# Kernel tuning notes

Hardware: AMD Instinct MI355X
Metric: run time of the kernel (lower is better)

## Reference

```python
import jax, jax.numpy as jnp
import numpy as np

# Dims
B, S, D = 2, 2048, 1024
H, KV = 16, 4            # rosa heads / kv heads -> n_rep = 4
QKB, VB = 16, 32          # query-key bits / value bits
N_REP = H // KV
TAU = 1.0


def setup_inputs() -> dict:
    key = jax.random.key(0)
    ks = jax.random.split(key, 8)
    sc = lambda fan_in: 1.0 / np.sqrt(fan_in)
    return {
        "hidden_states": jax.random.normal(ks[0], (B, S, D), jnp.float32),
        # Linear weights stored (in, out) so y = x @ W
        "Wq": jax.random.normal(ks[1], (D, H * QKB), jnp.float32) * sc(D),
        "Wk": jax.random.normal(ks[2], (D, KV * QKB), jnp.float32) * sc(D),
        "Wv": jax.random.normal(ks[3], (D, KV * VB), jnp.float32) * sc(D),
        "Wo": jax.random.normal(ks[4], (H * VB, D), jnp.float32) * sc(H * VB),
        "v_emb0": jnp.full((H * VB,), -1e-05, jnp.float32),
        "v_emb1": jnp.full((H * VB,), +1e-05, jnp.float32),
    }


def _repeat_kv(x, n_rep):
    # x: [B, KV, S, d] -> [B, KV*n_rep, S, d]
    b, kv, s, d = x.shape
    return jnp.broadcast_to(x[:, :, None], (b, kv, n_rep, s, d)).reshape(b, kv * n_rep, s, d)


def reference(hidden_states, Wq, Wk, Wv, Wo, v_emb0, v_emb1):
    b, s, _ = hidden_states.shape
    q = (hidden_states @ Wq).reshape(b, s, H, QKB).transpose(0, 2, 1, 3)   # [B,H,S,QKB]
    k = (hidden_states @ Wk).reshape(b, s, KV, QKB).transpose(0, 2, 1, 3)
    v = (hidden_states @ Wv).reshape(b, s, KV, VB).transpose(0, 2, 1, 3)
    k = _repeat_kv(k, N_REP)                                               # [B,H,S,QKB]
    v = _repeat_kv(v, N_REP)                                               # [B,H,S,VB]

    # Soft binarization (hard path uses (x > 0); soft path relaxes with sigmoid(x/tau)).
    pq = jax.nn.sigmoid(q / TAU)
    pk = jax.nn.sigmoid(k / TAU)
    pv = jax.nn.sigmoid(v / TAU)

    # Expected number of matching bits between soft-binary q_i and k_j:
    # sum_b [ pq*pk + (1-pq)(1-pk) ] = QKB - sum(pq) - sum(pk) + 2 * pq.pk
    dot = jnp.einsum("bhsd,bhtd->bhst", pq, pk)                            # [B,H,S,S]
    scores = QKB - pq.sum(-1)[:, :, :, None] - pk.sum(-1)[:, :, None, :] + 2.0 * dot

    causal = jnp.tril(jnp.ones((s, s), bool))                              # [S,S]
    scores = jnp.where(causal[None, None], scores, jnp.finfo(scores.dtype).min)
    attn = jax.nn.softmax(scores / TAU, axis=-1)

    vh = jnp.einsum("bhst,bhtd->bhsd", attn, pv)                           # [B,H,S,VB]
    e0 = v_emb0.reshape(1, H, 1, VB)
    e1 = v_emb1.reshape(1, H, 1, VB)
    out = e0 * (1.0 - vh) + e1 * vh                                        # [B,H,S,VB]
    out = out.transpose(0, 2, 1, 3).reshape(b, s, H * VB)
    return out @ Wo                                                        # [B,S,D]
```

## Files before the change

### kernel.cpp

```cpp
#include <hip/hip_runtime.h>
#include <hip/hip_bf16.h>

#define B_    2
#define S_    2048
#define D_    1024
#define H_    16
#define KV_   4
#define QKB_  16
#define VB_   32
#define NTOK  (B_ * S_)
#define L2E_  1.44269504088896f

typedef __attribute__((ext_vector_type(8))) short bshort8;
typedef __attribute__((ext_vector_type(4))) float f32x4;

__device__ __forceinline__ unsigned short bf16_rne(float x) {
    unsigned u = __float_as_uint(x);
    return (unsigned short)((u + 0x7FFFu + ((u >> 16) & 1u)) >> 16);
}
__device__ __forceinline__ unsigned bf16x2_rne(float lo, float hi) {
    return (unsigned)bf16_rne(lo) | ((unsigned)bf16_rne(hi) << 16);
}
__device__ __forceinline__ unsigned cvt_pk_bf16(float lo, float hi) {
    unsigned r;
    asm("v_cvt_pk_bf16_f32 %0, %1, %2" : "=v"(r) : "v"(lo), "v"(hi));
    return r;
}
__device__ __forceinline__ float sum2bf(unsigned u) {
    return __uint_as_float(u << 16) + __uint_as_float(u & 0xFFFF0000u);
}
__device__ __forceinline__ void stage16(const unsigned short* g, unsigned short* l) {
    __builtin_amdgcn_global_load_lds(
        (const __attribute__((address_space(1))) void*)g,
        (__attribute__((address_space(3))) void*)l, 16, 0, 0);
}

__global__ __launch_bounds__(256) void prep_kernel(
    const float* __restrict__ hs,
    const float* __restrict__ Wq, const float* __restrict__ Wk,
    const float* __restrict__ Wv, const float* __restrict__ Wo,
    unsigned short* __restrict__ hs_b,
    unsigned short* __restrict__ Wcat_t, unsigned short* __restrict__ Wot)
{
    __shared__ float T[64][65];
    const int t = threadIdx.x;
    if (blockIdx.x < 2048) {
        int i = blockIdx.x * 256 + t;
        const float4* s = (const float4*)hs;
        float4 a = s[2 * i], b = s[2 * i + 1];
        uint4 o;
        o.x = bf16x2_rne(a.x, a.y); o.y = bf16x2_rne(a.z, a.w);
        o.z = bf16x2_rne(b.x, b.y); o.w = bf16x2_rne(b.z, b.w);
        ((uint4*)hs_b)[i] = o;
        return;
    }
    const int bid = blockIdx.x - 2048;
    const float* src; unsigned short* dst; int K, N, tk, tn, drow0;
    if (bid < 64)       { src = Wq; dst = Wcat_t; K = 1024; N = 256;  int r = bid;       tk = r & 15; tn = r >> 4; drow0 = 0; }
    else if (bid < 80)  { src = Wk; dst = Wcat_t; K = 1024; N = 64;   int r = bid - 64;  tk = r;      tn = 0;      drow0 = 256; }
    else if (bid < 112) { src = Wv; dst = Wcat_t; K = 1024; N = 128;  int r = bid - 80;  tk = r & 15; tn = r >> 4; drow0 = 320; }
    else                { src = Wo; dst = Wot;    K = 512;  N = 1024; int r = bid - 112; tk = r & 7;  tn = r >> 3; drow0 = 0; }
    const int k0 = tk * 64, n0 = tn * 64;
    const int rr = t >> 4, cc = (t & 15) * 4;
    #pragma unroll
    for (int i = 0; i < 4; ++i) {
        float4 v = *(const float4*)(src + (k0 + rr + i * 16) * N + n0 + cc);
        T[rr + i * 16][cc + 0] = v.x; T[rr + i * 16][cc + 1] = v.y;
        T[rr + i * 16][cc + 2] = v.z; T[rr + i * 16][cc + 3] = v.w;
    }
    __syncthreads();
    const int nloc = t >> 2, kc = (t & 3) * 16;
    unsigned o[8];
    #pragma unroll
    for (int j = 0; j < 8; ++j)
        o[j] = bf16x2_rne(T[kc + 2 * j][nloc], T[kc + 2 * j + 1][nloc]);
    unsigned short* dp = dst + (drow0 + n0 + nloc) * K + k0 + kc;
    uint4 w0; w0.x = o[0]; w0.y = o[1]; w0.z = o[2]; w0.w = o[3];
    uint4 w1; w1.x = o[4]; w1.y = o[5]; w1.z = o[6]; w1.w = o[7];
    *(uint4*)(dp) = w0;
    *(uint4*)(dp + 8) = w1;
}

__global__ __launch_bounds__(256, 4) void proj_gemm(
    const unsigned short* __restrict__ Ab, const unsigned short* __restrict__ Btb,
    unsigned short* __restrict__ qg, unsigned short* __restrict__ pko,
    unsigned short* __restrict__ pvT)
{
    __shared__ unsigned short As[64 * 64];
    __shared__ unsigned short Bs[64 * 64];
    const int tid = threadIdx.x, l = tid & 63, w = tid >> 6;
    const int l15 = l & 15, quad = l >> 4;
    const int m0 = blockIdx.x * 64, n0 = blockIdx.y * 64;
    const int sr8 = l >> 3, sc8 = l & 7;
    f32x4 c[4];
    #pragma unroll
    for (int j = 0; j < 4; ++j) c[j] = (f32x4){0.f, 0.f, 0.f, 0.f};

    for (int k0 = 0; k0 < 1024; k0 += 64) {
        int R0 = w * 8, r0 = R0 + sr8;
        int R1 = 32 + w * 8, r1 = R1 + sr8;
        stage16(Ab  + (m0 + r0) * 1024 + k0 + (sc8 ^ (r0 & 7)) * 8, &As[R0 * 64]);
        stage16(Ab  + (m0 + r1) * 1024 + k0 + (sc8 ^ (r1 & 7)) * 8, &As[R1 * 64]);
        stage16(Btb + (n0 + r0) * 1024 + k0 + (sc8 ^ (r0 & 7)) * 8, &Bs[R0 * 64]);
        stage16(Btb + (n0 + r1) * 1024 + k0 + (sc8 ^ (r1 & 7)) * 8, &Bs[R1 * 64]);
        __syncthreads();
        #pragma unroll
        for (int kh = 0; kh < 2; ++kh) {
            const int arow = w * 16 + l15;
            bshort8 a = *(const bshort8*)&As[arow * 64 + (((kh * 4 + quad) ^ (arow & 7)) * 8)];
            #pragma unroll
            for (int bc = 0; bc < 4; ++bc) {
                const int brow = bc * 16 + l15;
                bshort8 b = *(const bshort8*)&Bs[brow * 64 + (((kh * 4 + quad) ^ (brow & 7)) * 8)];
                c[bc] = __builtin_amdgcn_mfma_f32_16x16x32_bf16(a, b, c[bc], 0, 0, 0);
            }
        }
        __syncthreads();
    }

    const int tok0 = m0 + w * 16 + quad * 4;
    #pragma unroll
    for (int bc = 0; bc < 4; ++bc) {
        f32x4 v = c[bc];
        const int n = n0 + bc * 16 + l15;
        float sg[4];
        #pragma unroll
        for (int r = 0; r < 4; ++r)
            sg[r] = 1.f / (1.f + exp2f(-v[r] * L2E_));
        if (n < 256) {
            const int hh = n >> 4, d = n & 15;
            #pragma unroll
            for (int r = 0; r < 4; ++r) {
                int tok = tok0 + r, bb = tok >> 11, ss = tok & 2047;
                qg[(((bb * 16 + hh) * 2048) + ss) * 16 + d] =
                    bf16_rne(L2E_ * (2.f * sg[r] - 1.f));
            }
        } else if (n < 320) {
            const int j = n - 256, kvv = j >> 4, d = j & 15;
            #pragma unroll
            for (int r = 0; r < 4; ++r) {
                int tok = tok0 + r, bb = tok >> 11, ss = tok & 2047;
                pko[(((bb * 4 + kvv) * 2048) + ss) * 16 + d] = bf16_rne(sg[r]);
            }
        } else {
            const int j = n - 320, kvv = j >> 5, d = j & 31;
            const int bb = tok0 >> 11, ss = tok0 & 2047;
            const int tl = ss >> 6, ccol = ss & 63;
            uint2 wv; wv.x = bf16x2_rne(sg[0], sg[1]); wv.y = bf16x2_rne(sg[2], sg[3]);
            *(uint2*)(pvT + ((((bb * 4 + kvv) * 32) + tl) * 32 + d) * 64 + ccol) = wv;
        }
    }
}

__global__ __launch_bounds__(256, 2) void outproj_gemm(
    const unsigned short* __restrict__ Ab, const unsigned short* __restrict__ Btb,
    float* __restrict__ out)
{
    __shared__ unsigned short As[64 * 64];
    __shared__ unsigned short Bs[128 * 64];
    const int tid = threadIdx.x, l = tid & 63, w = tid >> 6;
    const int l15 = l & 15, quad = l >> 4;
    const int m0 = blockIdx.x * 64, n0 = blockIdx.y * 128;
    const int wr = w & 1, wc = w >> 1;
    const int sr8 = l >> 3, sc8 = l & 7;
    f32x4 c[2][4];
    #pragma unroll
    for (int i = 0; i < 2; ++i)
        #pragma unroll
        for (int j = 0; j < 4; ++j) c[i][j] = (f32x4){0.f, 0.f, 0.f, 0.f};

    for (int k0 = 0; k0 < 512; k0 += 64) {
        #pragma unroll
        for (int j = 0; j < 2; ++j) {
            int R = w * 16 + j * 8, r = R + sr8;
            stage16(Ab + (m0 + r) * 512 + k0 + (sc8 ^ (r & 7)) * 8, &As[R * 64]);
        }
        #pragma unroll
        for (int j = 0; j < 4; ++j) {
            int R = j * 32 + w * 8, r = R + sr8;
            stage16(Btb + (n0 + r) * 512 + k0 + (sc8 ^ (r & 7)) * 8, &Bs[R * 64]);
        }
        __syncthreads();
        #pragma unroll
        for (int kh = 0; kh < 2; ++kh) {
            bshort8 a[2], b[4];
            #pragma unroll
            for (int ar = 0; ar < 2; ++ar) {
                int row = wr * 32 + ar * 16 + l15;
                a[ar] = *(const bshort8*)&As[row * 64 + (((kh * 4 + quad) ^ (row & 7)) * 8)];
            }
            #pragma unroll
            for (int bc = 0; bc < 4; ++bc) {
                int row = wc * 64 + bc * 16 + l15;
                b[bc] = *(const bshort8*)&Bs[row * 64 + (((kh * 4 + quad) ^ (row & 7)) * 8)];
            }
            #pragma unroll
            for (int ar = 0; ar < 2; ++ar)
                #pragma unroll
                for (int bc = 0; bc < 4; ++bc)
                    c[ar][bc] = __builtin_amdgcn_mfma_f32_16x16x32_bf16(a[ar], b[bc], c[ar][bc], 0, 0, 0);
        }
        __syncthreads();
    }

    #pragma unroll
    for (int ar = 0; ar < 2; ++ar)
        #pragma unroll
        for (int bc = 0; bc < 4; ++bc) {
            f32x4 v = c[ar][bc];
            const int col = n0 + wc * 64 + bc * 16 + l15;
            const int r0 = m0 + wr * 32 + ar * 16 + quad * 4;
            #pragma unroll
            for (int r = 0; r < 4; ++r)
                out[(r0 + r) * D_ + col] = v[r];
        }
}

__global__ __launch_bounds__(256, 4) void attn_kernel(
    const unsigned short* __restrict__ qg_g, const unsigned short* __restrict__ pk_g,
    const unsigned short* __restrict__ pvT_g, const float* __restrict__ e0,
    const float* __restrict__ e1, unsigned short* __restrict__ xo)
{
    __shared__ unsigned short P[4][16][88];
    const int tid = threadIdx.x, l = tid & 63, wq = tid >> 6;
    const int l15 = l & 15, quad = l >> 4;
    const int g = blockIdx.x;
    const int idx = g & 255, kg = g >> 8;
    const int bh = idx & 31, rr = idx >> 5;
    int qt;
    if      (kg == 0) qt = rr;
    else if (kg == 1) qt = 31 - rr;
    else if (kg == 2) qt = 8 + rr;
    else              qt = 23 - rr;
    const int b = bh >> 4, h = bh & 15, kv = h >> 2;
    const int qbase = qt * 64;
    const unsigned short* pkb = pk_g + ((b * 4 + kv) * 2048) * 16;
    const unsigned short* pvb = pvT_g + (b * 4 + kv) * 65536;
    const unsigned short* qgb = qg_g + ((b * 16 + h) * 2048) * 16;

    const f32x4 zero4 = {0.f, 0.f, 0.f, 0.f};
    const bshort8 zero8 = {0, 0, 0, 0, 0, 0, 0, 0};

    const unsigned short* qrow = qgb + (qbase + wq * 16 + l15) * 16;
    uint4 qu0 = *(const uint4*)qrow;
    uint4 qu1 = *(const uint4*)(qrow + 8);
    float s = sum2bf(qu0.x) + sum2bf(qu0.y) + sum2bf(qu0.z) + sum2bf(qu0.w)
            + sum2bf(qu1.x) + sum2bf(qu1.y) + sum2bf(qu1.z) + sum2bf(qu1.w);
    bshort8 qfrag = zero8;
    if (quad == 0)      qfrag = __builtin_bit_cast(bshort8, qu0);
    else if (quad == 1) qfrag = __builtin_bit_cast(bshort8, qu1);
    else if (quad == 2) qfrag[0] = (short)bf16_rne(-8.f * L2E_ - 0.5f * s);

    bshort8 kone = zero8; kone[0] = (short)0x3F80;

    f32x4 acc0 = zero4, acc1 = zero4;
    float lsum = 0.f;

    bshort8 kc[4], vc[4], kn[4], vn[4];
    if (quad < 2) {
        #pragma unroll
        for (int ks = 0; ks < 4; ++ks)
            kc[ks] = *(const bshort8*)(pkb + (ks * 16 + l15) * 16 + quad * 8);
    }
    {
        const unsigned short* vb = pvb + l15 * 64 + quad * 8;
        vc[0] = *(const bshort8*)(vb);
        vc[1] = *(const bshort8*)(vb + 32);
        vc[2] = *(const bshort8*)(vb + 1024);
        vc[3] = *(const bshort8*)(vb + 1056);
    }

    #pragma unroll 2
    for (int t = 0; t < qt; ++t) {
        if (quad < 2) {
            #pragma unroll
            for (int ks = 0; ks < 4; ++ks)
                kn[ks] = *(const bshort8*)(pkb + ((t + 1) * 64 + ks * 16 + l15) * 16 + quad * 8);
        }
        {
            const unsigned short* vb = pvb + (t + 1) * 2048 + l15 * 64 + quad * 8;
            vn[0] = *(const bshort8*)(vb);
            vn[1] = *(const bshort8*)(vb + 32);
            vn[2] = *(const bshort8*)(vb + 1024);
            vn[3] = *(const bshort8*)(vb + 1056);
        }
        f32x4 sc[4];
        #pragma unroll
        for (int ks = 0; ks < 4; ++ks) {
            bshort8 kf;
            if (quad < 2)       kf = kc[ks];
            else if (quad == 2) kf = kone;
            else                kf = zero8;
            sc[ks] = __builtin_amdgcn_mfma_f32_16x16x32_bf16(kf, qfrag, zero4, 0, 0, 0);
        }
        #pragma unroll
        for (int ks = 0; ks < 4; ++ks) {
            float p0 = exp2f(sc[ks][0]), p1 = exp2f(sc[ks][1]);
            float p2 = exp2f(sc[ks][2]), p3 = exp2f(sc[ks][3]);
            lsum += p0 + p1 + p2 + p3;
            uint2 wv; wv.x = cvt_pk_bf16(p0, p1); wv.y = cvt_pk_bf16(p2, p3);
            *(uint2*)&P[wq][l15][ks * 16 + quad * 4] = wv;
        }
        {
            bshort8 pf0 = *(const bshort8*)&P[wq][l15][quad * 8];
            bshort8 pf1 = *(const bshort8*)&P[wq][l15][32 + quad * 8];
            acc0 = __builtin_amdgcn_mfma_f32_16x16x32_bf16(vc[0], pf0, acc0, 0, 0, 0);
            acc1 = __builtin_amdgcn_mfma_f32_16x16x32_bf16(vc[2], pf0, acc1, 0, 0, 0);
            acc0 = __builtin_amdgcn_mfma_f32_16x16x32_bf16(vc[1], pf1, acc0, 0, 0, 0);
            acc1 = __builtin_amdgcn_mfma_f32_16x16x32_bf16(vc[3], pf1, acc1, 0, 0, 0);
        }
        #pragma unroll
        for (int i = 0; i < 4; ++i) { kc[i] = kn[i]; vc[i] = vn[i]; }
    }

    {
        const int t0 = qt * 64;
        const int q_lane = qbase + wq * 16 + l15;
        f32x4 sc[4];
        #pragma unroll
        for (int ks = 0; ks < 4; ++ks) {
            bshort8 kf;
            if (quad < 2)       kf = kc[ks];
            else if (quad == 2) kf = kone;
            else                kf = zero8;
            sc[ks] = __builtin_amdgcn_mfma_f32_16x16x32_bf16(kf, qfrag, zero4, 0, 0, 0);
        }
        #pragma unroll
        for (int ks = 0; ks < 4; ++ks) {
            float pv0[4];
            #pragma unroll
            for (int r = 0; r < 4; ++r) {
                const int tg = t0 + ks * 16 + quad * 4 + r;
                float pp = (tg <= q_lane) ? exp2f(sc[ks][r]) : 0.f;
                lsum += pp; pv0[r] = pp;
            }
            uint2 wv; wv.x = cvt_pk_bf16(pv0[0], pv0[1]); wv.y = cvt_pk_bf16(pv0[2], pv0[3]);
            *(uint2*)&P[wq][l15][ks * 16 + quad * 4] = wv;
        }
        {
            bshort8 pf0 = *(const bshort8*)&P[wq][l15][quad * 8];
            bshort8 pf1 = *(const bshort8*)&P[wq][l15][32 + quad * 8];
            acc0 = __builtin_amdgcn_mfma_f32_16x16x32_bf16(vc[0], pf0, acc0, 0, 0, 0);
            acc1 = __builtin_amdgcn_mfma_f32_16x16x32_bf16(vc[2], pf0, acc1, 0, 0, 0);
            acc0 = __builtin_amdgcn_mfma_f32_16x16x32_bf16(vc[1], pf1, acc0, 0, 0, 0);
            acc1 = __builtin_amdgcn_mfma_f32_16x16x32_bf16(vc[3], pf1, acc1, 0, 0, 0);
        }
    }

    lsum += __shfl_xor(lsum, 16);
    lsum += __shfl_xor(lsum, 32);
    const float inv = 1.f / lsum;

    float e0v[8], dEv[8];
    #pragma unroll
    for (int vs = 0; vs < 2; ++vs)
        #pragma unroll
        for (int r = 0; r < 4; ++r) {
            int idx2 = h * 32 + vs * 16 + quad * 4 + r;
            float a = e0[idx2];
            e0v[vs * 4 + r] = a; dEv[vs * 4 + r] = e1[idx2] - a;
        }
    const int tok = b * 2048 + qbase + wq * 16 + l15;
    float o0[4], o1[4];
    #pragma unroll
    for (int r = 0; r < 4; ++r) {
        o0[r] = e0v[r]     + dEv[r]     * (acc0[r] * inv);
        o1[r] = e0v[4 + r] + dEv[4 + r] * (acc1[r] * inv);
    }
    uint2 w0; w0.x = cvt_pk_bf16(o0[0], o0[1]); w0.y = cvt_pk_bf16(o0[2], o0[3]);
    uint2 w1; w1.x = cvt_pk_bf16(o1[0], o1[1]); w1.y = cvt_pk_bf16(o1[2], o1[3]);
    *(uint2*)(xo + tok * 512 + h * 32 + quad * 4)      = w0;
    *(uint2*)(xo + tok * 512 + h * 32 + 16 + quad * 4) = w1;
}

extern "C" void kernel_launch(void* const* d_in, const int* in_sizes, int n_in,
                              void* d_out, int out_size, void* d_ws, size_t ws_size,
                              hipStream_t stream)
{
    const float* hs = (const float*)d_in[0];
    const float* Wq = (const float*)d_in[1];
    const float* Wk = (const float*)d_in[2];
    const float* Wv = (const float*)d_in[3];
    const float* Wo = (const float*)d_in[4];
    const float* e0 = (const float*)d_in[5];
    const float* e1 = (const float*)d_in[6];
    float* out = (float*)d_out;

    char* ws = (char*)d_ws;
    unsigned short* hs_b   = (unsigned short*)(ws);
    unsigned short* xo     = (unsigned short*)(ws);
    unsigned short* Wcat_t = (unsigned short*)(ws + 8388608);
    unsigned short* Wot    = (unsigned short*)(ws + 8388608 + 917504);
    unsigned short* qg     = (unsigned short*)(ws + 10354688);
    unsigned short* pk     = (unsigned short*)(ws + 12451840);
    unsigned short* pvT    = (unsigned short*)(ws + 12976128);

    prep_kernel<<<2288, 256, 0, stream>>>(hs, Wq, Wk, Wv, Wo, hs_b, Wcat_t, Wot);
    proj_gemm<<<dim3(64, 7), 256, 0, stream>>>(hs_b, Wcat_t, qg, pk, pvT);
    attn_kernel<<<1024, 256, 0, stream>>>(qg, pk, pvT, e0, e1, xo);
    outproj_gemm<<<dim3(64, 8), 256, 0, stream>>>(xo, Wot, out);
}
```

Baseline: 145.0 us.

## Split attention key range across two blocks and merge partials in finalize kernel

Each query tile's causal key range is divided into two halves processed by separate blocks, doubling the attention grid. Each block writes unnormalized fp32 accumulators and row sums to workspace. A new finalize kernel adds the two halves, normalizes, applies the value embeddings and writes bf16 output. This aims to improve load balance and parallelism, at the cost of extra global memory traffic for partials and an additional kernel launch.

```diff
diff --git a/kernel.cpp b/kernel.cpp
--- a/kernel.cpp
+++ b/kernel.cpp
@@ -218,20 +218,22 @@
 
 __global__ __launch_bounds__(256, 4) void attn_kernel(
     const unsigned short* __restrict__ qg_g, const unsigned short* __restrict__ pk_g,
-    const unsigned short* __restrict__ pvT_g, const float* __restrict__ e0,
-    const float* __restrict__ e1, unsigned short* __restrict__ xo)
+    const unsigned short* __restrict__ pvT_g,
+    float* __restrict__ pacc, float* __restrict__ plsum)
 {
     __shared__ unsigned short P[4][16][88];
     const int tid = threadIdx.x, l = tid & 63, wq = tid >> 6;
     const int l15 = l & 15, quad = l >> 4;
     const int g = blockIdx.x;
-    const int idx = g & 255, kg = g >> 8;
-    const int bh = idx & 31, rr = idx >> 5;
-    int qt;
-    if      (kg == 0) qt = rr;
-    else if (kg == 1) qt = 31 - rr;
-    else if (kg == 2) qt = 8 + rr;
-    else              qt = 23 - rr;
+    const int c = g & 255, j = g >> 8;
+    const int bh = c & 31, rr = c >> 5;
+    const int r = rr + ((j & 1) << 3);
+    const int hk = j >> 1;
+    const int qt = (hk & 2) ? (31 - r) : r;
+    const int half = hk & 1;
+    const int m = (qt + 1) >> 1;
+    const int kt0 = half ? m : 0;
+    const int nt  = half ? (qt - m) : m;
     const int b = bh >> 4, h = bh & 15, kv = h >> 2;
     const int qbase = qt * 64;
     const unsigned short* pkb = pk_g + ((b * 4 + kv) * 2048) * 16;
@@ -257,120 +259,140 @@
     float lsum = 0.f;
 
     bshort8 kc[4], vc[4], kn[4], vn[4];
-    if (quad < 2) {
-        #pragma unroll
-        for (int ks = 0; ks < 4; ++ks)
-            kc[ks] = *(const bshort8*)(pkb + (ks * 16 + l15) * 16 + quad * 8);
-    }
-    {
-        const unsigned short* vb = pvb + l15 * 64 + quad * 8;
-        vc[0] = *(const bshort8*)(vb);
-        vc[1] = *(const bshort8*)(vb + 32);
-        vc[2] = *(const bshort8*)(vb + 1024);
-        vc[3] = *(const bshort8*)(vb + 1056);
-    }
-
-    #pragma unroll 2
-    for (int t = 0; t < qt; ++t) {
+    if (nt > 0 || half) {
         if (quad < 2) {
             #pragma unroll
             for (int ks = 0; ks < 4; ++ks)
-                kn[ks] = *(const bshort8*)(pkb + ((t + 1) * 64 + ks * 16 + l15) * 16 + quad * 8);
+                kc[ks] = *(const bshort8*)(pkb + (kt0 * 64 + ks * 16 + l15) * 16 + quad * 8);
         }
         {
-            const unsigned short* vb = pvb + (t + 1) * 2048 + l15 * 64 + quad * 8;
-            vn[0] = *(const bshort8*)(vb);
-            vn[1] = *(const bshort8*)(vb + 32);
-            vn[2] = *(const bshort8*)(vb + 1024);
-            vn[3] = *(const bshort8*)(vb + 1056);
-        }
-        f32x4 sc[4];
-        #pragma unroll
-        for (int ks = 0; ks < 4; ++ks) {
-            bshort8 kf;
-            if (quad < 2)       kf = kc[ks];
-            else if (quad == 2) kf = kone;
-            else                kf = zero8;
-            sc[ks] = __builtin_amdgcn_mfma_f32_16x16x32_bf16(kf, qfrag, zero4, 0, 0, 0);
-        }
-        #pragma unroll
-        for (int ks = 0; ks < 4; ++ks) {
-            float p0 = exp2f(sc[ks][0]), p1 = exp2f(sc[ks][1]);
-            float p2 = exp2f(sc[ks][2]), p3 = exp2f(sc[ks][3]);
-            lsum += p0 + p1 + p2 + p3;
-            uint2 wv; wv.x = cvt_pk_bf16(p0, p1); wv.y = cvt_pk_bf16(p2, p3);
-            *(uint2*)&P[wq][l15][ks * 16 + quad * 4] = wv;
-        }
-        {
-            bshort8 pf0 = *(const bshort8*)&P[wq][l15][quad * 8];
-            bshort8 pf1 = *(const bshort8*)&P[wq][l15][32 + quad * 8];
-            acc0 = __builtin_amdgcn_mfma_f32_16x16x32_bf16(vc[0], pf0, acc0, 0, 0, 0);
-            acc1 = __builtin_amdgcn_mfma_f32_16x16x32_bf16(vc[2], pf0, acc1, 0, 0, 0);
-            acc0 = __builtin_amdgcn_mfma_f32_16x16x32_bf16(vc[1], pf1, acc0, 0, 0, 0);
-            acc1 = __builtin_amdgcn_mfma_f32_16x16x32_bf16(vc[3], pf1, acc1, 0, 0, 0);
-        }
-        #pragma unroll
-        for (int i = 0; i < 4; ++i) { kc[i] = kn[i]; vc[i] = vn[i]; }
-    }
-
-    {
-        const int t0 = qt * 64;
-        const int q_lane = qbase + wq * 16 + l15;
-        f32x4 sc[4];
-        #pragma unroll
-        for (int ks = 0; ks < 4; ++ks) {
-            bshort8 kf;
-            if (quad < 2)       kf = kc[ks];
-            else if (quad == 2) kf = kone;
-            else                kf = zero8;
-            sc[ks] = __builtin_amdgcn_mfma_f32_16x16x32_bf16(kf, qfrag, zero4, 0, 0, 0);
-        }
-        #pragma unroll
-        for (int ks = 0; ks < 4; ++ks) {
-            float pv0[4];
-            #pragma unroll
-            for (int r = 0; r < 4; ++r) {
-                const int tg = t0 + ks * 16 + quad * 4 + r;
-                float pp = (tg <= q_lane) ? exp2f(sc[ks][r]) : 0.f;
-                lsum += pp; pv0[r] = pp;
-            }
-            uint2 wv; wv.x = cvt_pk_bf16(pv0[0], pv0[1]); wv.y = cvt_pk_bf16(pv0[2], pv0[3]);
-            *(uint2*)&P[wq][l15][ks * 16 + quad * 4] = wv;
-        }
-        {
-            bshort8 pf0 = *(const bshort8*)&P[wq][l15][quad * 8];
-            bshort8 pf1 = *(const bshort8*)&P[wq][l15][32 + quad * 8];
-            acc0 = __builtin_amdgcn_mfma_f32_16x16x32_bf16(vc[0], pf0, acc0, 0, 0, 0);
-            acc1 = __builtin_amdgcn_mfma_f32_16x16x32_bf16(vc[2], pf0, acc1, 0, 0, 0);
-            acc0 = __builtin_amdgcn_mfma_f32_16x16x32_bf16(vc[1], pf1, acc0, 0, 0, 0);
-            acc1 = __builtin_amdgcn_mfma_f32_16x16x32_bf16(vc[3], pf1, acc1, 0, 0, 0);
+            const unsigned short* vb = pvb + kt0 * 2048 + l15 * 64 + quad * 8;
+            vc[0] = *(const bshort8*)(vb);
+            vc[1] = *(const bshort8*)(vb + 32);
+            vc[2] = *(const bshort8*)(vb + 1024);
+            vc[3] = *(const bshort8*)(vb + 1056);
+        }
+
+        #pragma unroll 2
+        for (int t = 0; t < nt; ++t) {
+            if (quad < 2) {
+                #pragma unroll
+                for (int ks = 0; ks < 4; ++ks)
+                    kn[ks] = *(const bshort8*)(pkb + ((kt0 + t + 1) * 64 + ks * 16 + l15) * 16 + quad * 8);
+            }
+            {
+                const unsigned short* vb = pvb + (kt0 + t + 1) * 2048 + l15 * 64 + quad * 8;
+                vn[0] = *(const bshort8*)(vb);
+                vn[1] = *(const bshort8*)(vb + 32);
+                vn[2] = *(const bshort8*)(vb + 1024);
+                vn[3] = *(const bshort8*)(vb + 1056);
+            }
+            f32x4 sc[4];
+            #pragma unroll
+            for (int ks = 0; ks < 4; ++ks) {
+                bshort8 kf;
+                if (quad < 2)       kf = kc[ks];
+                else if (quad == 2) kf = kone;
+                else                kf = zero8;
+                sc[ks] = __builtin_amdgcn_mfma_f32_16x16x32_bf16(kf, qfrag, zero4, 0, 0, 0);
+            }
+            #pragma unroll
+            for (int ks = 0; ks < 4; ++ks) {
+                float p0 = exp2f(sc[ks][0]), p1 = exp2f(sc[ks][1]);
+                float p2 = exp2f(sc[ks][2]), p3 = exp2f(sc[ks][3]);
+                lsum += p0 + p1 + p2 + p3;
+                uint2 wv; wv.x = cvt_pk_bf16(p0, p1); wv.y = cvt_pk_bf16(p2, p3);
+                *(uint2*)&P[wq][l15][ks * 16 + quad * 4] = wv;
+            }
+            {
+                bshort8 pf0 = *(const bshort8*)&P[wq][l15][quad * 8];
+                bshort8 pf1 = *(const bshort8*)&P[wq][l15][32 + quad * 8];
+                acc0 = __builtin_amdgcn_mfma_f32_16x16x32_bf16(vc[0], pf0, acc0, 0, 0, 0);
+                acc1 = __builtin_amdgcn_mfma_f32_16x16x32_bf16(vc[2], pf0, acc1, 0, 0, 0);
+                acc0 = __builtin_amdgcn_mfma_f32_16x16x32_bf16(vc[1], pf1, acc0, 0, 0, 0);
+                acc1 = __builtin_amdgcn_mfma_f32_16x16x32_bf16(vc[3], pf1, acc1, 0, 0, 0);
+            }
+            #pragma unroll
+            for (int i = 0; i < 4; ++i) { kc[i] = kn[i]; vc[i] = vn[i]; }
+        }
+
+        if (half) {
+            const int t0 = qt * 64;
+            const int q_lane = qbase + wq * 16 + l15;
+            f32x4 sc[4];
+            #pragma unroll
+            for (int ks = 0; ks < 4; ++ks) {
+                bshort8 kf;
+                if (quad < 2)       kf = kc[ks];
+                else if (quad == 2) kf = kone;
+                else                kf = zero8;
+                sc[ks] = __builtin_amdgcn_mfma_f32_16x16x32_bf16(kf, qfrag, zero4, 0, 0, 0);
+            }
+            #pragma unroll
+            for (int ks = 0; ks < 4; ++ks) {
+                float pv0[4];
+                #pragma unroll
+                for (int r2 = 0; r2 < 4; ++r2) {
+                    const int tg = t0 + ks * 16 + quad * 4 + r2;
+                    float pp = (tg <= q_lane) ? exp2f(sc[ks][r2]) : 0.f;
+                    lsum += pp; pv0[r2] = pp;
+                }
+                uint2 wv; wv.x = cvt_pk_bf16(pv0[0], pv0[1]); wv.y = cvt_pk_bf16(pv0[2], pv0[3]);
+                *(uint2*)&P[wq][l15][ks * 16 + quad * 4] = wv;
+            }
+            {
+                bshort8 pf0 = *(const bshort8*)&P[wq][l15][quad * 8];
+                bshort8 pf1 = *(const bshort8*)&P[wq][l15][32 + quad * 8];
+                acc0 = __builtin_amdgcn_mfma_f32_16x16x32_bf16(vc[0], pf0, acc0, 0, 0, 0);
+                acc1 = __builtin_amdgcn_mfma_f32_16x16x32_bf16(vc[2], pf0, acc1, 0, 0, 0);
+                acc0 = __builtin_amdgcn_mfma_f32_16x16x32_bf16(vc[1], pf1, acc0, 0, 0, 0);
+                acc1 = __builtin_amdgcn_mfma_f32_16x16x32_bf16(vc[3], pf1, acc1, 0, 0, 0);
+            }
         }
     }
 
     lsum += __shfl_xor(lsum, 16);
     lsum += __shfl_xor(lsum, 32);
-    const float inv = 1.f / lsum;
-
-    float e0v[8], dEv[8];
-    #pragma unroll
-    for (int vs = 0; vs < 2; ++vs)
-        #pragma unroll
-        for (int r = 0; r < 4; ++r) {
-            int idx2 = h * 32 + vs * 16 + quad * 4 + r;
-            float a = e0[idx2];
-            e0v[vs * 4 + r] = a; dEv[vs * 4 + r] = e1[idx2] - a;
-        }
-    const int tok = b * 2048 + qbase + wq * 16 + l15;
-    float o0[4], o1[4];
-    #pragma unroll
-    for (int r = 0; r < 4; ++r) {
-        o0[r] = e0v[r]     + dEv[r]     * (acc0[r] * inv);
-        o1[r] = e0v[4 + r] + dEv[4 + r] * (acc1[r] * inv);
-    }
-    uint2 w0; w0.x = cvt_pk_bf16(o0[0], o0[1]); w0.y = cvt_pk_bf16(o0[2], o0[3]);
-    uint2 w1; w1.x = cvt_pk_bf16(o1[0], o1[1]); w1.y = cvt_pk_bf16(o1[2], o1[3]);
-    *(uint2*)(xo + tok * 512 + h * 32 + quad * 4)      = w0;
-    *(uint2*)(xo + tok * 512 + h * 32 + 16 + quad * 4) = w1;
+    const int jobid = (bh * 32 + qt) * 2 + half;
+    float* pa = pacc + (jobid * 64 + wq * 16 + l15) * 32;
+    *(float4*)(pa + quad * 4)      = *(float4*)&acc0;
+    *(float4*)(pa + 16 + quad * 4) = *(float4*)&acc1;
+    if (quad == 0) plsum[jobid * 64 + wq * 16 + l15] = lsum;
+}
+
+__global__ __launch_bounds__(256) void attn_fin(
+    const float* __restrict__ pacc, const float* __restrict__ plsum,
+    const float* __restrict__ e0, const float* __restrict__ e1,
+    unsigned short* __restrict__ xo)
+{
+    const int g = blockIdx.x;
+    const int bh = g >> 5, qt = g & 31;
+    const int b = bh >> 4, h = bh & 15;
+    const int t = threadIdx.x, row = t >> 2, vg = t & 3;
+    const int j0 = g * 2;
+    const float ls = plsum[j0 * 64 + row] + plsum[j0 * 64 + 64 + row];
+    const float inv = 1.f / ls;
+    const float* a0 = pacc + (j0 * 64 + row) * 32 + vg * 8;
+    const float* a1 = pacc + ((j0 + 1) * 64 + row) * 32 + vg * 8;
+    float4 x0 = ((const float4*)a0)[0], x1 = ((const float4*)a0)[1];
+    float4 y0 = ((const float4*)a1)[0], y1 = ((const float4*)a1)[1];
+    const int base = h * 32 + vg * 8;
+    float sv[8];
+    sv[0] = (x0.x + y0.x) * inv; sv[1] = (x0.y + y0.y) * inv;
+    sv[2] = (x0.z + y0.z) * inv; sv[3] = (x0.w + y0.w) * inv;
+    sv[4] = (x1.x + y1.x) * inv; sv[5] = (x1.y + y1.y) * inv;
+    sv[6] = (x1.z + y1.z) * inv; sv[7] = (x1.w + y1.w) * inv;
+    float o[8];
+    #pragma unroll
+    for (int k = 0; k < 8; ++k) {
+        float a = e0[base + k];
+        o[k] = a + (e1[base + k] - a) * sv[k];
+    }
+    uint4 uv;
+    uv.x = cvt_pk_bf16(o[0], o[1]); uv.y = cvt_pk_bf16(o[2], o[3]);
+    uv.z = cvt_pk_bf16(o[4], o[5]); uv.w = cvt_pk_bf16(o[6], o[7]);
+    const int tok = b * 2048 + qt * 64 + row;
+    *(uint4*)(xo + tok * 512 + h * 32 + vg * 8) = uv;
 }
 
 extern "C" void kernel_launch(void* const* d_in, const int* in_sizes, int n_in,
@@ -394,9 +416,12 @@
     unsigned short* qg     = (unsigned short*)(ws + 10354688);
     unsigned short* pk     = (unsigned short*)(ws + 12451840);
     unsigned short* pvT    = (unsigned short*)(ws + 12976128);
+    float*          pacc   = (float*)(ws + 16777216);
+    float*          plsum  = (float*)(ws + 33554432);
 
     prep_kernel<<<2288, 256, 0, stream>>>(hs, Wq, Wk, Wv, Wo, hs_b, Wcat_t, Wot);
     proj_gemm<<<dim3(64, 7), 256, 0, stream>>>(hs_b, Wcat_t, qg, pk, pvT);
-    attn_kernel<<<1024, 256, 0, stream>>>(qg, pk, pvT, e0, e1, xo);
+    attn_kernel<<<2048, 256, 0, stream>>>(qg, pk, pvT, pacc, plsum);
+    attn_fin<<<1024, 256, 0, stream>>>(pacc, plsum, e0, e1, xo);
     outproj_gemm<<<dim3(64, 8), 256, 0, stream>>>(xo, Wot, out);
 }
```

New measurement: 155.7 us. 7.4% more time.

## Stage K/V tiles cooperatively in swizzled shared memory instead of per-wave registers

Applied to the files above, without the earlier changes.

Each block's 256 threads now load every K and V tile into shared memory once, with an XOR swizzle on V, and all four waves read their MFMA fragments from there. Before, each wave loaded the same tiles from global memory into registers. The diagonal (masked) tile is folded into the main loop under a branch. This removes the redundant per-wave global loads, at the cost of two block barriers per tile and the loss of the register double-buffered prefetch that overlapped the next tile's loads with compute.

```diff
diff --git a/kernel.cpp b/kernel.cpp
--- a/kernel.cpp
+++ b/kernel.cpp
@@ -221,6 +221,8 @@
     const unsigned short* __restrict__ pvT_g, const float* __restrict__ e0,
     const float* __restrict__ e1, unsigned short* __restrict__ xo)
 {
+    __shared__ unsigned short Ks[64 * 16];
+    __shared__ unsigned short Vs[32 * 64];
     __shared__ unsigned short P[4][16][88];
     const int tid = threadIdx.x, l = tid & 63, wq = tid >> 6;
     const int l15 = l & 15, quad = l >> 4;
@@ -256,95 +258,70 @@
     f32x4 acc0 = zero4, acc1 = zero4;
     float lsum = 0.f;
 
-    bshort8 kc[4], vc[4], kn[4], vn[4];
-    if (quad < 2) {
-        #pragma unroll
-        for (int ks = 0; ks < 4; ++ks)
-            kc[ks] = *(const bshort8*)(pkb + (ks * 16 + l15) * 16 + quad * 8);
-    }
-    {
-        const unsigned short* vb = pvb + l15 * 64 + quad * 8;
-        vc[0] = *(const bshort8*)(vb);
-        vc[1] = *(const bshort8*)(vb + 32);
-        vc[2] = *(const bshort8*)(vb + 1024);
-        vc[3] = *(const bshort8*)(vb + 1056);
-    }
-
-    #pragma unroll 2
-    for (int t = 0; t < qt; ++t) {
-        if (quad < 2) {
-            #pragma unroll
-            for (int ks = 0; ks < 4; ++ks)
-                kn[ks] = *(const bshort8*)(pkb + ((t + 1) * 64 + ks * 16 + l15) * 16 + quad * 8);
-        }
-        {
-            const unsigned short* vb = pvb + (t + 1) * 2048 + l15 * 64 + quad * 8;
-            vn[0] = *(const bshort8*)(vb);
-            vn[1] = *(const bshort8*)(vb + 32);
-            vn[2] = *(const bshort8*)(vb + 1024);
-            vn[3] = *(const bshort8*)(vb + 1056);
-        }
+    const int vrow_s = tid >> 3;
+    const unsigned short* vsrc = pvb + vrow_s * 64 + (((tid & 7) ^ (vrow_s & 7)) * 8);
+    unsigned short* vdst = &Vs[tid * 8];
+    const unsigned short* ksrc = pkb + (tid >> 1) * 16 + (tid & 1) * 8;
+    unsigned short* kdst = &Ks[tid * 8];
+
+    const int koff = l15 * 16 + quad * 8;
+    const int vx0 = ((quad ^ (l15 & 7)) * 8);
+    const int vx1 = (((quad + 4) ^ (l15 & 7)) * 8);
+    const int vrow = l15 * 64;
+
+    const int q_lane = qbase + wq * 16 + l15;
+
+    for (int t = 0; t <= qt; ++t) {
+        stage16(vsrc + t * 2048, vdst);
+        if (tid < 128) stage16(ksrc + t * 1024, kdst);
+        __syncthreads();
+
         f32x4 sc[4];
         #pragma unroll
         for (int ks = 0; ks < 4; ++ks) {
             bshort8 kf;
-            if (quad < 2)       kf = kc[ks];
+            if (quad < 2)       kf = *(const bshort8*)&Ks[ks * 256 + koff];
             else if (quad == 2) kf = kone;
             else                kf = zero8;
             sc[ks] = __builtin_amdgcn_mfma_f32_16x16x32_bf16(kf, qfrag, zero4, 0, 0, 0);
         }
-        #pragma unroll
-        for (int ks = 0; ks < 4; ++ks) {
-            float p0 = exp2f(sc[ks][0]), p1 = exp2f(sc[ks][1]);
-            float p2 = exp2f(sc[ks][2]), p3 = exp2f(sc[ks][3]);
-            lsum += p0 + p1 + p2 + p3;
-            uint2 wv; wv.x = cvt_pk_bf16(p0, p1); wv.y = cvt_pk_bf16(p2, p3);
-            *(uint2*)&P[wq][l15][ks * 16 + quad * 4] = wv;
+        if (t < qt) {
+            #pragma unroll
+            for (int ks = 0; ks < 4; ++ks) {
+                float p0 = exp2f(sc[ks][0]), p1 = exp2f(sc[ks][1]);
+                float p2 = exp2f(sc[ks][2]), p3 = exp2f(sc[ks][3]);
+                lsum += p0 + p1 + p2 + p3;
+                uint2 wv; wv.x = cvt_pk_bf16(p0, p1); wv.y = cvt_pk_bf16(p2, p3);
+                *(uint2*)&P[wq][l15][ks * 16 + quad * 4] = wv;
+            }
+        } else {
+            const int t0 = qt * 64;
+            #pragma unroll
+            for (int ks = 0; ks < 4; ++ks) {
+                float pv0[4];
+                #pragma unroll
+                for (int r = 0; r < 4; ++r) {
+                    const int tg = t0 + ks * 16 + quad * 4 + r;
+                    float pp = (tg <= q_lane) ? exp2f(sc[ks][r]) : 0.f;
+                    lsum += pp; pv0[r] = pp;
+                }
+                uint2 wv; wv.x = cvt_pk_bf16(pv0[0], pv0[1]); wv.y = cvt_pk_bf16(pv0[2], pv0[3]);
+                *(uint2*)&P[wq][l15][ks * 16 + quad * 4] = wv;
+            }
         }
         {
             bshort8 pf0 = *(const bshort8*)&P[wq][l15][quad * 8];
             bshort8 pf1 = *(const bshort8*)&P[wq][l15][32 + quad * 8];
-            acc0 = __builtin_amdgcn_mfma_f32_16x16x32_bf16(vc[0], pf0, acc0, 0, 0, 0);
-            acc1 = __builtin_amdgcn_mfma_f32_16x16x32_bf16(vc[2], pf0, acc1, 0, 0, 0);
-            acc0 = __builtin_amdgcn_mfma_f32_16x16x32_bf16(vc[1], pf1, acc0, 0, 0, 0);
-            acc1 = __builtin_amdgcn_mfma_f32_16x16x32_bf16(vc[3], pf1, acc1, 0, 0, 0);
-        }
-        #pragma unroll
-        for (int i = 0; i < 4; ++i) { kc[i] = kn[i]; vc[i] = vn[i]; }
-    }
-
-    {
-        const int t0 = qt * 64;
-        const int q_lane = qbase + wq * 16 + l15;
-        f32x4 sc[4];
-        #pragma unroll
-        for (int ks = 0; ks < 4; ++ks) {
-            bshort8 kf;
-            if (quad < 2)       kf = kc[ks];
-            else if (quad == 2) kf = kone;
-            else                kf = zero8;
-            sc[ks] = __builtin_amdgcn_mfma_f32_16x16x32_bf16(kf, qfrag, zero4, 0, 0, 0);
-        }
-        #pragma unroll
-        for (int ks = 0; ks < 4; ++ks) {
-            float pv0[4];
-            #pragma unroll
-            for (int r = 0; r < 4; ++r) {
-                const int tg = t0 + ks * 16 + quad * 4 + r;
-                float pp = (tg <= q_lane) ? exp2f(sc[ks][r]) : 0.f;
-                lsum += pp; pv0[r] = pp;
-            }
-            uint2 wv; wv.x = cvt_pk_bf16(pv0[0], pv0[1]); wv.y = cvt_pk_bf16(pv0[2], pv0[3]);
-            *(uint2*)&P[wq][l15][ks * 16 + quad * 4] = wv;
-        }
-        {
-            bshort8 pf0 = *(const bshort8*)&P[wq][l15][quad * 8];
-            bshort8 pf1 = *(const bshort8*)&P[wq][l15][32 + quad * 8];
-            acc0 = __builtin_amdgcn_mfma_f32_16x16x32_bf16(vc[0], pf0, acc0, 0, 0, 0);
-            acc1 = __builtin_amdgcn_mfma_f32_16x16x32_bf16(vc[2], pf0, acc1, 0, 0, 0);
-            acc0 = __builtin_amdgcn_mfma_f32_16x16x32_bf16(vc[1], pf1, acc0, 0, 0, 0);
-            acc1 = __builtin_amdgcn_mfma_f32_16x16x32_bf16(vc[3], pf1, acc1, 0, 0, 0);
-        }
+            bshort8 v0 = *(const bshort8*)&Vs[vrow + vx0];
+            bshort8 v1 = *(const bshort8*)&Vs[vrow + vx1];
+            bshort8 v2 = *(const bshort8*)&Vs[vrow + 1024 + vx0];
+            bshort8 v3 = *(const bshort8*)&Vs[vrow + 1024 + vx1];
+            acc0 = __builtin_amdgcn_mfma_f32_16x16x32_bf16(v0, pf0, acc0, 0, 0, 0);
+            acc1 = __builtin_amdgcn_mfma_f32_16x16x32_bf16(v2, pf0, acc1, 0, 0, 0);
+            acc0 = __builtin_amdgcn_mfma_f32_16x16x32_bf16(v1, pf1, acc0, 0, 0, 0);
+            acc1 = __builtin_amdgcn_mfma_f32_16x16x32_bf16(v3, pf1, acc1, 0, 0, 0);
+        }
+        __syncthreads();
     }
 
     lsum += __shfl_xor(lsum, 16);
```

Result: faster. 138.1 us (-4.8%).
